# Performance work log

Hardware: AMD Instinct MI355X
Metric: run time of the kernel (lower is better)

The kernel has to match this reference:

```python
import jax, jax.numpy as jnp
import numpy as np

N_NODES = 100000
N_EDGES = 1600000


def setup_inputs() -> dict:
    key = jax.random.key(0)
    k1, k2, k3, k4 = jax.random.split(key, 4)
    x = jax.random.normal(k1, (N_NODES, 128), dtype=jnp.float32)
    edge_index = jax.random.randint(k2, (2, N_EDGES), 0, N_NODES, dtype=jnp.int64)
    # Glorot-ish init for weights
    W1 = jax.random.normal(k3, (128, 128), dtype=jnp.float32) * (1.0 / np.sqrt(128))
    b1 = jnp.zeros((128,), dtype=jnp.float32)
    W2 = jax.random.normal(k4, (128, 64), dtype=jnp.float32) * (1.0 / np.sqrt(128))
    b2 = jnp.zeros((64,), dtype=jnp.float32)
    return {"x": x, "edge_index": edge_index, "W1": W1, "b1": b1, "W2": W2, "b2": b2}


def _gcn_conv(x, src, dst, W, b):
    """PyG GCNConv: h = W x; symmetric deg^-1/2 norm over edges (incl. self-loops); scatter-add; + bias."""
    n = x.shape[0]
    h = x @ W  # [N, out]
    ones = jnp.ones(src.shape[0], dtype=h.dtype)
    deg = jax.ops.segment_sum(ones, dst, num_segments=n)  # in-degree incl self-loops
    dinv = jax.lax.rsqrt(jnp.maximum(deg, 1e-12))
    norm = dinv[src] * dinv[dst]  # [E+N]
    msg = h[src] * norm[:, None]  # [E+N, out] gather
    out = jax.ops.segment_sum(msg, dst, num_segments=n)  # scatter-add
    return out + b


def reference(x, edge_index, W1, b1, W2, b2):
    n = x.shape[0]
    loop = jnp.arange(n, dtype=edge_index.dtype)
    src = jnp.concatenate([edge_index[0], loop])  # add self-loops
    dst = jnp.concatenate([edge_index[1], loop])
    h = jax.nn.relu(_gcn_conv(x, src, dst, W1, b1))
    # dropout is identity in eval mode
    return _gcn_conv(h, src, dst, W2, b2)
```

## Files before the change

### kernel.cpp

```cpp
#include <hip/hip_runtime.h>
#include <hip/hip_bf16.h>

#define THREADS 256
#define BSHIFT 9
#define BIN_CHUNK 4096

typedef __attribute__((ext_vector_type(8))) short bf16x8;
typedef __attribute__((ext_vector_type(4))) float f32x4;


__device__ inline unsigned short f2bf(float f) {
    unsigned int u = __float_as_uint(f);
    unsigned int r = (u + 0x7fffu + ((u >> 16) & 1u)) >> 16;
    return (unsigned short)r;
}

__device__ inline unsigned int pack_bf2(float x, float y) {
    return (unsigned int)f2bf(x) | ((unsigned int)f2bf(y) << 16);
}

__device__ inline float2 bf2_to_f2(unsigned int u) {
    float2 r;
    r.x = __uint_as_float(u << 16);
    r.y = __uint_as_float(u & 0xffff0000u);
    return r;
}

__device__ inline unsigned short bf_relu(unsigned short v) {
    return (v & 0x8000u) ? (unsigned short)0 : v;
}

__device__ inline void accum_row(float* acc, uint4 v) {
    float2 a = bf2_to_f2(v.x), b = bf2_to_f2(v.y), c = bf2_to_f2(v.z), d = bf2_to_f2(v.w);
    acc[0] += a.x; acc[1] += a.y; acc[2] += b.x; acc[3] += b.y;
    acc[4] += c.x; acc[5] += c.y; acc[6] += d.x; acc[7] += d.y;
}


__global__ __launch_bounds__(256) void k_bin(const int* __restrict__ src,
                                             const int* __restrict__ dst,
                                             int* __restrict__ bcur,
                                             unsigned int* __restrict__ binned,
                                             int E, int NB, int cap) {
    __shared__ int bcnt[256];
    __shared__ int bres[256];
    int t = threadIdx.x;
    bcnt[t] = 0;
    __syncthreads();
    int base = blockIdx.x * BIN_CHUNK;
    int sv[16], dv[16];
#pragma unroll
    for (int i = 0; i < 16; ++i) {
        int e = base + t + i * 256;
        if (e < E) {
            sv[i] = src[e];
            dv[i] = dst[e];
            atomicAdd(&bcnt[dv[i] >> BSHIFT], 1);
        } else {
            dv[i] = -1;
        }
    }
    __syncthreads();
    if (t < NB) {
        int old = bcnt[t] ? atomicAdd(&bcur[t], bcnt[t]) : 0;
        bres[t] = t * cap + old;
    }
    __syncthreads();
#pragma unroll
    for (int i = 0; i < 16; ++i) {
        if (dv[i] >= 0) {
            int b = dv[i] >> BSHIFT;
            int pos = atomicAdd(&bres[b], 1);
            if (pos < (b + 1) * cap)
                binned[pos] = ((unsigned int)(dv[i] & 511) << 23) | (unsigned int)sv[i];
        }
    }
}

__global__ __launch_bounds__(256) void k_node_place(const unsigned int* __restrict__ binned,
                                                    const int* __restrict__ bcur, int cap,
                                                    int* __restrict__ rp,
                                                    int* __restrict__ deg,
                                                    float* __restrict__ dinv,
                                                    int* __restrict__ eperm, int N) {
    __shared__ int lc[512];
    __shared__ int s[256];
    int b = blockIdx.x;
    int t = threadIdx.x;
    int beg = b * cap;
    int end = beg + min(bcur[b], cap);
    int d0 = b << BSHIFT;
    lc[t] = 0;
    lc[t + 256] = 0;
    __syncthreads();
    for (int j = beg + t; j < end; j += 256) atomicAdd(&lc[binned[j] >> 23], 1);
    __syncthreads();
    int a = lc[2 * t], c = lc[2 * t + 1];
    int pair = a + c;
    s[t] = pair;
    __syncthreads();
    for (int off = 1; off < 256; off <<= 1) {
        int add = (t >= off) ? s[t - off] : 0;
        __syncthreads();
        s[t] += add;
        __syncthreads();
    }
    int excl = s[t] - pair;
    int st0 = beg + excl, st1 = st0 + a;
    int node0 = d0 + 2 * t;
    if (node0 < N) {
        rp[node0] = st0;
        deg[node0] = a;
        dinv[node0] = rsqrtf((float)a + 1.0f);
    }
    if (node0 + 1 < N) {
        rp[node0 + 1] = st1;
        deg[node0 + 1] = c;
        dinv[node0 + 1] = rsqrtf((float)c + 1.0f);
    }
    __syncthreads();
    lc[2 * t] = st0;
    lc[2 * t + 1] = st1;
    __syncthreads();
    for (int j = beg + t; j < end; j += 256) {
        unsigned int p = binned[j];
        int pos = atomicAdd(&lc[p >> 23], 1);
        eperm[pos] = (int)(p & 0x7fffffu);
    }
}


template <int N, bool ABF16_RELU>
__global__ __launch_bounds__(256) void k_gemm_mfma(const void* __restrict__ Av,
                                                   const float* __restrict__ W,
                                                   const float* __restrict__ dinv,
                                                   unsigned short* __restrict__ C, int M) {
    static_assert(N == 64 || N == 128, "N must be 64 or 128");
    constexpr int NT = N / 64;
    constexpr int KP = 136;
    __shared__ short As[64 * KP];
    __shared__ short Bs[N * KP];
    __shared__ float sDin[64];

    const int t = threadIdx.x;
    const int m0 = blockIdx.x * 64;

    {
        int ar = t >> 5;
        int ac = (t & 31) * 4;
#pragma unroll
        for (int rb = 0; rb < 64; rb += 8) {
            int lrow = rb + ar;
            int row = m0 + lrow;
            ushort4 sv = make_ushort4(0, 0, 0, 0);
            if (ABF16_RELU) {
                if (row < M) {
                    ushort4 u = *(const ushort4*)((const unsigned short*)Av + (size_t)row * 128 + ac);
                    sv.x = bf_relu(u.x); sv.y = bf_relu(u.y);
                    sv.z = bf_relu(u.z); sv.w = bf_relu(u.w);
                }
            } else {
                if (row < M) {
                    float4 v = *(const float4*)((const float*)Av + (size_t)row * 128 + ac);
                    sv.x = f2bf(v.x); sv.y = f2bf(v.y); sv.z = f2bf(v.z); sv.w = f2bf(v.w);
                }
            }
            *(ushort4*)&As[lrow * KP + ac] = sv;
        }
    }
    {
        constexpr int TPR = N / 4;
        constexpr int KPI = 256 / TPR;
        int bk = t / TPR;
        int bn = (t % TPR) * 4;
#pragma unroll
        for (int kb = 0; kb < 128; kb += KPI) {
            int k = kb + bk;
            float4 wv = *(const float4*)(W + (size_t)k * N + bn);
            Bs[(bn + 0) * KP + k] = f2bf(wv.x);
            Bs[(bn + 1) * KP + k] = f2bf(wv.y);
            Bs[(bn + 2) * KP + k] = f2bf(wv.z);
            Bs[(bn + 3) * KP + k] = f2bf(wv.w);
        }
    }
    if (t < 64) sDin[t] = (m0 + t < M) ? dinv[m0 + t] : 1.0f;
    __syncthreads();

    const int w = t >> 6;
    const int lane = t & 63;
    const int lm = lane & 15;
    const int qd = lane >> 4;
    const int n0w = w * 16 * NT;

    f32x4 acc[4][NT];
#pragma unroll
    for (int mi = 0; mi < 4; ++mi)
#pragma unroll
        for (int ni = 0; ni < NT; ++ni) acc[mi][ni] = (f32x4){0.f, 0.f, 0.f, 0.f};

#pragma unroll
    for (int ks = 0; ks < 4; ++ks) {
        bf16x8 a[4], b[NT];
#pragma unroll
        for (int mi = 0; mi < 4; ++mi)
            a[mi] = *(const bf16x8*)&As[(mi * 16 + lm) * KP + ks * 32 + qd * 8];
#pragma unroll
        for (int ni = 0; ni < NT; ++ni)
            b[ni] = *(const bf16x8*)&Bs[(n0w + ni * 16 + lm) * KP + ks * 32 + qd * 8];
#pragma unroll
        for (int mi = 0; mi < 4; ++mi)
#pragma unroll
            for (int ni = 0; ni < NT; ++ni)
                acc[mi][ni] = __builtin_amdgcn_mfma_f32_16x16x32_bf16(a[mi], b[ni], acc[mi][ni], 0, 0, 0);
    }

#pragma unroll
    for (int mi = 0; mi < 4; ++mi) {
#pragma unroll
        for (int ni = 0; ni < NT; ++ni) {
            int col = n0w + ni * 16 + lm;
#pragma unroll
            for (int r = 0; r < 4; ++r) {
                int lrow = mi * 16 + qd * 4 + r;
                int row = m0 + lrow;
                if (row < M) C[(size_t)row * N + col] = f2bf(sDin[lrow] * acc[mi][ni][r]);
            }
        }
    }
}


__global__ __launch_bounds__(256) void k_gather128(const int* __restrict__ rp,
                                                   const int* __restrict__ deg,
                                                   const int* __restrict__ eperm,
                                                   const float* __restrict__ dinv,
                                                   const uint4* __restrict__ h4,
                                                   const float* __restrict__ bias,
                                                   uint4* __restrict__ out4,
                                                   int n) {
    const int t = threadIdx.x;
    const int lane = t & 63;
    const int l16 = lane & 15;
    const int gbase = lane & 48;
    const int node = blockIdx.x * 16 + (t >> 6) * 4 + (lane >> 4);
    const bool valid = node < n;

    int beg = 0, end = 0;
    if (valid) {
        beg = rp[node];
        end = beg + deg[node];
    }

    float acc[8];
#pragma unroll
    for (int i = 0; i < 8; ++i) acc[i] = 0.f;
    if (valid) accum_row(acc, h4[(size_t)node * 16 + l16]);

    int j = beg;
    for (; j + 16 <= end; j += 16) {
        int ep = eperm[j + l16];
        int idx[16];
#pragma unroll
        for (int k = 0; k < 16; ++k) idx[k] = __shfl(ep, gbase + k);
        uint4 v[16];
#pragma unroll
        for (int k = 0; k < 16; ++k) v[k] = h4[(size_t)idx[k] * 16 + l16];
#pragma unroll
        for (int k = 0; k < 16; ++k) accum_row(acc, v[k]);
    }
    int cnt = end - j;
    if (cnt > 0) {
        int ep = eperm[j + (l16 < cnt ? l16 : cnt - 1)];
        int k = 0;
        for (; k + 4 <= cnt; k += 4) {
            int i0 = __shfl(ep, gbase + k);
            int i1 = __shfl(ep, gbase + k + 1);
            int i2 = __shfl(ep, gbase + k + 2);
            int i3 = __shfl(ep, gbase + k + 3);
            uint4 v0 = h4[(size_t)i0 * 16 + l16];
            uint4 v1 = h4[(size_t)i1 * 16 + l16];
            uint4 v2 = h4[(size_t)i2 * 16 + l16];
            uint4 v3 = h4[(size_t)i3 * 16 + l16];
            accum_row(acc, v0);
            accum_row(acc, v1);
            accum_row(acc, v2);
            accum_row(acc, v3);
        }
        for (; k < cnt; ++k) {
            int i0 = __shfl(ep, gbase + k);
            uint4 v0 = h4[(size_t)i0 * 16 + l16];
            accum_row(acc, v0);
        }
    }

    if (valid) {
        float dv = dinv[node];
        float4 b0 = ((const float4*)bias)[l16 * 2];
        float4 b1 = ((const float4*)bias)[l16 * 2 + 1];
        uint4 o;
        o.x = pack_bf2(dv * acc[0] + b0.x, dv * acc[1] + b0.y);
        o.y = pack_bf2(dv * acc[2] + b0.z, dv * acc[3] + b0.w);
        o.z = pack_bf2(dv * acc[4] + b1.x, dv * acc[5] + b1.y);
        o.w = pack_bf2(dv * acc[6] + b1.z, dv * acc[7] + b1.w);
        out4[(size_t)node * 16 + l16] = o;
    }
}

__global__ __launch_bounds__(256) void k_gather64(const int* __restrict__ rp,
                                                  const int* __restrict__ deg,
                                                  const int* __restrict__ eperm,
                                                  const float* __restrict__ dinv,
                                                  const uint4* __restrict__ h4,
                                                  const float* __restrict__ bias,
                                                  float* __restrict__ out, int n) {
    const int t = threadIdx.x;
    const int lane = t & 63;
    const int l8 = lane & 7;
    const int gbase = lane & 56;
    const int node = blockIdx.x * 32 + (t >> 6) * 8 + (lane >> 3);
    const bool valid = node < n;

    int beg = 0, end = 0;
    if (valid) {
        beg = rp[node];
        end = beg + deg[node];
    }

    float acc[8];
#pragma unroll
    for (int i = 0; i < 8; ++i) acc[i] = 0.f;
    if (valid) accum_row(acc, h4[(size_t)node * 8 + l8]);

    int j = beg;
    for (; j + 16 <= end; j += 16) {
        int ep0 = eperm[j + l8];
        int ep1 = eperm[j + 8 + l8];
        int idx[16];
#pragma unroll
        for (int k = 0; k < 8; ++k) idx[k] = __shfl(ep0, gbase + k);
#pragma unroll
        for (int k = 0; k < 8; ++k) idx[8 + k] = __shfl(ep1, gbase + k);
        uint4 v[16];
#pragma unroll
        for (int k = 0; k < 16; ++k) v[k] = h4[(size_t)idx[k] * 8 + l8];
#pragma unroll
        for (int k = 0; k < 16; ++k) accum_row(acc, v[k]);
    }
    int cnt = end - j;
    if (cnt >= 8) {
        int ep = eperm[j + l8];
        int idx[8];
#pragma unroll
        for (int k = 0; k < 8; ++k) idx[k] = __shfl(ep, gbase + k);
        uint4 v[8];
#pragma unroll
        for (int k = 0; k < 8; ++k) v[k] = h4[(size_t)idx[k] * 8 + l8];
#pragma unroll
        for (int k = 0; k < 8; ++k) accum_row(acc, v[k]);
        j += 8;
        cnt -= 8;
    }
    if (cnt > 0) {
        int ep = eperm[j + (l8 < cnt ? l8 : cnt - 1)];
        int k = 0;
        for (; k + 4 <= cnt; k += 4) {
            int i0 = __shfl(ep, gbase + k);
            int i1 = __shfl(ep, gbase + k + 1);
            int i2 = __shfl(ep, gbase + k + 2);
            int i3 = __shfl(ep, gbase + k + 3);
            uint4 v0 = h4[(size_t)i0 * 8 + l8];
            uint4 v1 = h4[(size_t)i1 * 8 + l8];
            uint4 v2 = h4[(size_t)i2 * 8 + l8];
            uint4 v3 = h4[(size_t)i3 * 8 + l8];
            accum_row(acc, v0);
            accum_row(acc, v1);
            accum_row(acc, v2);
            accum_row(acc, v3);
        }
        for (; k < cnt; ++k) {
            int i0 = __shfl(ep, gbase + k);
            uint4 v0 = h4[(size_t)i0 * 8 + l8];
            accum_row(acc, v0);
        }
    }

    if (valid) {
        float dv = dinv[node];
        float4 b0 = ((const float4*)bias)[l8 * 2];
        float4 b1 = ((const float4*)bias)[l8 * 2 + 1];
        float4 o0, o1;
        o0.x = dv * acc[0] + b0.x; o0.y = dv * acc[1] + b0.y;
        o0.z = dv * acc[2] + b0.z; o0.w = dv * acc[3] + b0.w;
        o1.x = dv * acc[4] + b1.x; o1.y = dv * acc[5] + b1.y;
        o1.z = dv * acc[6] + b1.z; o1.w = dv * acc[7] + b1.w;
        float4* orow = (float4*)(out + (size_t)node * 64);
        orow[l8 * 2] = o0;
        orow[l8 * 2 + 1] = o1;
    }
}


extern "C" void kernel_launch(void* const* d_in, const int* in_sizes, int n_in,
                              void* d_out, int out_size, void* d_ws, size_t ws_size,
                              hipStream_t stream) {
    const float* x  = (const float*)d_in[0];
    const int*   ei = (const int*)d_in[1];
    const float* W1 = (const float*)d_in[2];
    const float* b1 = (const float*)d_in[3];
    const float* W2 = (const float*)d_in[4];
    const float* b2 = (const float*)d_in[5];
    float* out = (float*)d_out;

    const int N = in_sizes[0] / 128;
    const int E = in_sizes[1] / 2;
    const int* src = ei;
    const int* dst = ei + E;
    const int NB = (N + 511) >> BSHIFT;
    const int cap = (E + NB - 1) / NB + ((E / NB) >> 2) + 1024;

    char* ws = (char*)d_ws;
    size_t off = 0;
    auto carve = [&](size_t bytes) -> void* {
        void* p = ws + off;
        off = (off + bytes + 255) & ~(size_t)255;
        return p;
    };
    float* dinv = (float*)carve((size_t)N * 4);
    int*   rp   = (int*)carve((size_t)N * 4);
    int*   deg  = (int*)carve((size_t)N * 4);
    int*   bcur = (int*)carve(256 * 4);
    unsigned int* binned = (unsigned int*)carve((size_t)NB * cap * 4);
    int*   eperm = (int*)carve((size_t)NB * cap * 4);
    unsigned short* h    = (unsigned short*)carve((size_t)N * 128 * 2);
    unsigned short* hagg = (unsigned short*)carve((size_t)N * 128 * 2);
    unsigned short* h2 = h;

    const int gMm = (N + 63) / 64;

    hipMemsetAsync(bcur, 0, 256 * sizeof(int), stream);
    k_bin<<<(E + BIN_CHUNK - 1) / BIN_CHUNK, THREADS, 0, stream>>>(src, dst, bcur, binned, E, NB, cap);
    k_node_place<<<NB, THREADS, 0, stream>>>(binned, bcur, cap, rp, deg, dinv, eperm, N);

    k_gemm_mfma<128, false><<<gMm, THREADS, 0, stream>>>(x, W1, dinv, h, N);
    k_gather128<<<(N + 15) / 16, THREADS, 0, stream>>>(rp, deg, eperm, dinv, (const uint4*)h, b1,
                                                       (uint4*)hagg, N);

    k_gemm_mfma<64, true><<<gMm, THREADS, 0, stream>>>(hagg, W2, dinv, h2, N);
    k_gather64<<<(N + 31) / 32, THREADS, 0, stream>>>(rp, deg, eperm, dinv, (const uint4*)h2, b2, out, N);
}
```

Before: 290.9 us.

## Fuse edge binning with GEMM1 and layer-1 gather with GEMM2

Edge binning and the first dense transform now share one launch, so GEMM1 no longer depends on the degree computation. The transform output is left unscaled, and the per-source dinv is applied inside the gather via a per-edge scale. The layer-1 aggregation, ReLU and bias now write into shared memory and feed the second MFMA GEMM directly. This removes the hagg round trip through global memory and a launch, but adds an extra dinv gather per edge and lowers gather parallelism, since each block handles 64 nodes in a serial loop of four.

```diff
diff --git a/kernel.cpp b/kernel.cpp
--- a/kernel.cpp
+++ b/kernel.cpp
@@ -4,6 +4,7 @@
 #define THREADS 256
 #define BSHIFT 9
 #define BIN_CHUNK 4096
+#define KP 136
 
 typedef __attribute__((ext_vector_type(8))) short bf16x8;
 typedef __attribute__((ext_vector_type(4))) float f32x4;
@@ -13,10 +14,6 @@
     unsigned int u = __float_as_uint(f);
     unsigned int r = (u + 0x7fffu + ((u >> 16) & 1u)) >> 16;
     return (unsigned short)r;
-}
-
-__device__ inline unsigned int pack_bf2(float x, float y) {
-    return (unsigned int)f2bf(x) | ((unsigned int)f2bf(y) << 16);
 }
 
 __device__ inline float2 bf2_to_f2(unsigned int u) {
@@ -26,53 +23,142 @@
     return r;
 }
 
-__device__ inline unsigned short bf_relu(unsigned short v) {
-    return (v & 0x8000u) ? (unsigned short)0 : v;
-}
-
 __device__ inline void accum_row(float* acc, uint4 v) {
     float2 a = bf2_to_f2(v.x), b = bf2_to_f2(v.y), c = bf2_to_f2(v.z), d = bf2_to_f2(v.w);
     acc[0] += a.x; acc[1] += a.y; acc[2] += b.x; acc[3] += b.y;
     acc[4] += c.x; acc[5] += c.y; acc[6] += d.x; acc[7] += d.y;
 }
 
-
-__global__ __launch_bounds__(256) void k_bin(const int* __restrict__ src,
-                                             const int* __restrict__ dst,
-                                             int* __restrict__ bcur,
-                                             unsigned int* __restrict__ binned,
-                                             int E, int NB, int cap) {
-    __shared__ int bcnt[256];
-    __shared__ int bres[256];
-    int t = threadIdx.x;
-    bcnt[t] = 0;
-    __syncthreads();
-    int base = blockIdx.x * BIN_CHUNK;
-    int sv[16], dv[16];
-#pragma unroll
-    for (int i = 0; i < 16; ++i) {
-        int e = base + t + i * 256;
-        if (e < E) {
-            sv[i] = src[e];
-            dv[i] = dst[e];
-            atomicAdd(&bcnt[dv[i] >> BSHIFT], 1);
-        } else {
-            dv[i] = -1;
-        }
-    }
-    __syncthreads();
-    if (t < NB) {
-        int old = bcnt[t] ? atomicAdd(&bcur[t], bcnt[t]) : 0;
-        bres[t] = t * cap + old;
-    }
-    __syncthreads();
-#pragma unroll
-    for (int i = 0; i < 16; ++i) {
-        if (dv[i] >= 0) {
-            int b = dv[i] >> BSHIFT;
-            int pos = atomicAdd(&bres[b], 1);
-            if (pos < (b + 1) * cap)
-                binned[pos] = ((unsigned int)(dv[i] & 511) << 23) | (unsigned int)sv[i];
+__device__ inline void accum_row_scaled(float* acc, uint4 v, float s) {
+    float2 a = bf2_to_f2(v.x), b = bf2_to_f2(v.y), c = bf2_to_f2(v.z), d = bf2_to_f2(v.w);
+    acc[0] = fmaf(s, a.x, acc[0]); acc[1] = fmaf(s, a.y, acc[1]);
+    acc[2] = fmaf(s, b.x, acc[2]); acc[3] = fmaf(s, b.y, acc[3]);
+    acc[4] = fmaf(s, c.x, acc[4]); acc[5] = fmaf(s, c.y, acc[5]);
+    acc[6] = fmaf(s, d.x, acc[6]); acc[7] = fmaf(s, d.y, acc[7]);
+}
+
+
+__global__ __launch_bounds__(256) void k_bin_gemm1(const int* __restrict__ src,
+                                                   const int* __restrict__ dst,
+                                                   int* __restrict__ bcur,
+                                                   unsigned int* __restrict__ binned,
+                                                   int E, int NB, int cap,
+                                                   const float* __restrict__ x,
+                                                   const float* __restrict__ W1,
+                                                   unsigned short* __restrict__ h,
+                                                   int M, int nbin) {
+    __shared__ __align__(16) char smem[64 * KP * 2 + 128 * KP * 2];
+    const int t = threadIdx.x;
+
+    if ((int)blockIdx.x < nbin) {
+        int* bcnt = (int*)smem;
+        int* bres = bcnt + 256;
+        bcnt[t] = 0;
+        __syncthreads();
+        int base = blockIdx.x * BIN_CHUNK;
+        int sv[16], dv[16];
+#pragma unroll
+        for (int i = 0; i < 16; ++i) {
+            int e = base + t + i * 256;
+            if (e < E) {
+                sv[i] = src[e];
+                dv[i] = dst[e];
+                atomicAdd(&bcnt[dv[i] >> BSHIFT], 1);
+            } else {
+                dv[i] = -1;
+            }
+        }
+        __syncthreads();
+        if (t < NB) {
+            int old = bcnt[t] ? atomicAdd(&bcur[t], bcnt[t]) : 0;
+            bres[t] = t * cap + old;
+        }
+        __syncthreads();
+#pragma unroll
+        for (int i = 0; i < 16; ++i) {
+            if (dv[i] >= 0) {
+                int b = dv[i] >> BSHIFT;
+                int pos = atomicAdd(&bres[b], 1);
+                if (pos < (b + 1) * cap)
+                    binned[pos] = ((unsigned int)(dv[i] & 511) << 23) | (unsigned int)sv[i];
+            }
+        }
+        return;
+    }
+
+    short* As = (short*)smem;
+    short* Bs = (short*)(smem + 64 * KP * 2);
+    const int m0 = ((int)blockIdx.x - nbin) * 64;
+
+    {
+        int ar = t >> 5;
+        int ac = (t & 31) * 4;
+#pragma unroll
+        for (int rb = 0; rb < 64; rb += 8) {
+            int lrow = rb + ar;
+            int row = m0 + lrow;
+            ushort4 sv = make_ushort4(0, 0, 0, 0);
+            if (row < M) {
+                float4 v = *(const float4*)(x + (size_t)row * 128 + ac);
+                sv.x = f2bf(v.x); sv.y = f2bf(v.y); sv.z = f2bf(v.z); sv.w = f2bf(v.w);
+            }
+            *(ushort4*)&As[lrow * KP + ac] = sv;
+        }
+    }
+    {
+        int bk = t / 32;
+        int bn = (t % 32) * 4;
+#pragma unroll
+        for (int kb = 0; kb < 128; kb += 8) {
+            int k = kb + bk;
+            float4 wv = *(const float4*)(W1 + (size_t)k * 128 + bn);
+            Bs[(bn + 0) * KP + k] = f2bf(wv.x);
+            Bs[(bn + 1) * KP + k] = f2bf(wv.y);
+            Bs[(bn + 2) * KP + k] = f2bf(wv.z);
+            Bs[(bn + 3) * KP + k] = f2bf(wv.w);
+        }
+    }
+    __syncthreads();
+
+    const int w = t >> 6;
+    const int lane = t & 63;
+    const int lm = lane & 15;
+    const int qd = lane >> 4;
+    const int n0w = w * 32;
+
+    f32x4 acc[4][2];
+#pragma unroll
+    for (int mi = 0; mi < 4; ++mi)
+#pragma unroll
+        for (int ni = 0; ni < 2; ++ni) acc[mi][ni] = (f32x4){0.f, 0.f, 0.f, 0.f};
+
+#pragma unroll
+    for (int ks = 0; ks < 4; ++ks) {
+        bf16x8 a[4], b[2];
+#pragma unroll
+        for (int mi = 0; mi < 4; ++mi)
+            a[mi] = *(const bf16x8*)&As[(mi * 16 + lm) * KP + ks * 32 + qd * 8];
+#pragma unroll
+        for (int ni = 0; ni < 2; ++ni)
+            b[ni] = *(const bf16x8*)&Bs[(n0w + ni * 16 + lm) * KP + ks * 32 + qd * 8];
+#pragma unroll
+        for (int mi = 0; mi < 4; ++mi)
+#pragma unroll
+            for (int ni = 0; ni < 2; ++ni)
+                acc[mi][ni] = __builtin_amdgcn_mfma_f32_16x16x32_bf16(a[mi], b[ni], acc[mi][ni], 0, 0, 0);
+    }
+
+#pragma unroll
+    for (int mi = 0; mi < 4; ++mi) {
+#pragma unroll
+        for (int ni = 0; ni < 2; ++ni) {
+            int col = n0w + ni * 16 + lm;
+#pragma unroll
+            for (int r = 0; r < 4; ++r) {
+                int lrow = mi * 16 + qd * 4 + r;
+                int row = m0 + lrow;
+                if (row < M) h[(size_t)row * 128 + col] = f2bf(acc[mi][ni][r]);
+            }
         }
     }
 }
@@ -130,179 +216,138 @@
 }
 
 
-template <int N, bool ABF16_RELU>
-__global__ __launch_bounds__(256) void k_gemm_mfma(const void* __restrict__ Av,
-                                                   const float* __restrict__ W,
-                                                   const float* __restrict__ dinv,
-                                                   unsigned short* __restrict__ C, int M) {
-    static_assert(N == 64 || N == 128, "N must be 64 or 128");
-    constexpr int NT = N / 64;
-    constexpr int KP = 136;
+__global__ __launch_bounds__(256) void k_gather_gemm2(const int* __restrict__ rp,
+                                                      const int* __restrict__ deg,
+                                                      const int* __restrict__ eperm,
+                                                      const float* __restrict__ dinv,
+                                                      const uint4* __restrict__ h4,
+                                                      const float* __restrict__ b1,
+                                                      const float* __restrict__ W2,
+                                                      unsigned short* __restrict__ h2,
+                                                      int n) {
     __shared__ short As[64 * KP];
-    __shared__ short Bs[N * KP];
+    __shared__ short Bs[64 * KP];
     __shared__ float sDin[64];
 
     const int t = threadIdx.x;
+    const int lane = t & 63;
+    const int l16 = lane & 15;
+    const int gbase = lane & 48;
     const int m0 = blockIdx.x * 64;
 
     {
-        int ar = t >> 5;
-        int ac = (t & 31) * 4;
-#pragma unroll
-        for (int rb = 0; rb < 64; rb += 8) {
-            int lrow = rb + ar;
-            int row = m0 + lrow;
-            ushort4 sv = make_ushort4(0, 0, 0, 0);
-            if (ABF16_RELU) {
-                if (row < M) {
-                    ushort4 u = *(const ushort4*)((const unsigned short*)Av + (size_t)row * 128 + ac);
-                    sv.x = bf_relu(u.x); sv.y = bf_relu(u.y);
-                    sv.z = bf_relu(u.z); sv.w = bf_relu(u.w);
-                }
-            } else {
-                if (row < M) {
-                    float4 v = *(const float4*)((const float*)Av + (size_t)row * 128 + ac);
-                    sv.x = f2bf(v.x); sv.y = f2bf(v.y); sv.z = f2bf(v.z); sv.w = f2bf(v.w);
-                }
-            }
-            *(ushort4*)&As[lrow * KP + ac] = sv;
-        }
-    }
-    {
-        constexpr int TPR = N / 4;
-        constexpr int KPI = 256 / TPR;
-        int bk = t / TPR;
-        int bn = (t % TPR) * 4;
-#pragma unroll
-        for (int kb = 0; kb < 128; kb += KPI) {
+        int bk = t / 16;
+        int bn = (t % 16) * 4;
+#pragma unroll
+        for (int kb = 0; kb < 128; kb += 16) {
             int k = kb + bk;
-            float4 wv = *(const float4*)(W + (size_t)k * N + bn);
+            float4 wv = *(const float4*)(W2 + (size_t)k * 64 + bn);
             Bs[(bn + 0) * KP + k] = f2bf(wv.x);
             Bs[(bn + 1) * KP + k] = f2bf(wv.y);
             Bs[(bn + 2) * KP + k] = f2bf(wv.z);
             Bs[(bn + 3) * KP + k] = f2bf(wv.w);
         }
     }
-    if (t < 64) sDin[t] = (m0 + t < M) ? dinv[m0 + t] : 1.0f;
+    if (t < 64) sDin[t] = (m0 + t < n) ? dinv[m0 + t] : 1.0f;
+
+#pragma unroll 1
+    for (int r = 0; r < 4; ++r) {
+        const int lrow = r * 16 + ((t >> 6) << 2) + (lane >> 4);
+        const int node = m0 + lrow;
+        const bool valid = node < n;
+
+        int beg = 0, end = 0;
+        float dv_self = 0.f;
+        if (valid) {
+            beg = rp[node];
+            end = beg + deg[node];
+            dv_self = dinv[node];
+        }
+
+        float acc[8];
+#pragma unroll
+        for (int i = 0; i < 8; ++i) acc[i] = 0.f;
+        if (valid) accum_row_scaled(acc, h4[(size_t)node * 16 + l16], dv_self);
+
+        for (int j = beg; j < end; j += 16) {
+            int cnt = end - j;
+            if (cnt > 16) cnt = 16;
+            int ep = eperm[j + (l16 < cnt ? l16 : cnt - 1)];
+            float dvv = dinv[ep];
+            int k = 0;
+            for (; k + 4 <= cnt; k += 4) {
+                int i0 = __shfl(ep, gbase + k);
+                int i1 = __shfl(ep, gbase + k + 1);
+                int i2 = __shfl(ep, gbase + k + 2);
+                int i3 = __shfl(ep, gbase + k + 3);
+                float d0 = __shfl(dvv, gbase + k);
+                float d1 = __shfl(dvv, gbase + k + 1);
+                float d2 = __shfl(dvv, gbase + k + 2);
+                float d3 = __shfl(dvv, gbase + k + 3);
+                uint4 v0 = h4[(size_t)i0 * 16 + l16];
+                uint4 v1 = h4[(size_t)i1 * 16 + l16];
+                uint4 v2 = h4[(size_t)i2 * 16 + l16];
+                uint4 v3 = h4[(size_t)i3 * 16 + l16];
+                accum_row_scaled(acc, v0, d0);
+                accum_row_scaled(acc, v1, d1);
+                accum_row_scaled(acc, v2, d2);
+                accum_row_scaled(acc, v3, d3);
+            }
+            for (; k < cnt; ++k) {
+                int i0 = __shfl(ep, gbase + k);
+                float d0 = __shfl(dvv, gbase + k);
+                uint4 v0 = h4[(size_t)i0 * 16 + l16];
+                accum_row_scaled(acc, v0, d0);
+            }
+        }
+
+        float4 bb0 = ((const float4*)b1)[l16 * 2];
+        float4 bb1 = ((const float4*)b1)[l16 * 2 + 1];
+        float o0 = fmaxf(fmaf(dv_self, acc[0], bb0.x), 0.f);
+        float o1 = fmaxf(fmaf(dv_self, acc[1], bb0.y), 0.f);
+        float o2 = fmaxf(fmaf(dv_self, acc[2], bb0.z), 0.f);
+        float o3 = fmaxf(fmaf(dv_self, acc[3], bb0.w), 0.f);
+        float o4 = fmaxf(fmaf(dv_self, acc[4], bb1.x), 0.f);
+        float o5 = fmaxf(fmaf(dv_self, acc[5], bb1.y), 0.f);
+        float o6 = fmaxf(fmaf(dv_self, acc[6], bb1.z), 0.f);
+        float o7 = fmaxf(fmaf(dv_self, acc[7], bb1.w), 0.f);
+        ushort4 s0 = make_ushort4(f2bf(o0), f2bf(o1), f2bf(o2), f2bf(o3));
+        ushort4 s1 = make_ushort4(f2bf(o4), f2bf(o5), f2bf(o6), f2bf(o7));
+        *(ushort4*)&As[lrow * KP + l16 * 8] = s0;
+        *(ushort4*)&As[lrow * KP + l16 * 8 + 4] = s1;
+    }
     __syncthreads();
 
     const int w = t >> 6;
-    const int lane = t & 63;
     const int lm = lane & 15;
     const int qd = lane >> 4;
-    const int n0w = w * 16 * NT;
-
-    f32x4 acc[4][NT];
-#pragma unroll
-    for (int mi = 0; mi < 4; ++mi)
-#pragma unroll
-        for (int ni = 0; ni < NT; ++ni) acc[mi][ni] = (f32x4){0.f, 0.f, 0.f, 0.f};
+    const int n0w = w * 16;
+
+    f32x4 c4[4];
+#pragma unroll
+    for (int mi = 0; mi < 4; ++mi) c4[mi] = (f32x4){0.f, 0.f, 0.f, 0.f};
 
 #pragma unroll
     for (int ks = 0; ks < 4; ++ks) {
-        bf16x8 a[4], b[NT];
+        bf16x8 a[4], b;
 #pragma unroll
         for (int mi = 0; mi < 4; ++mi)
             a[mi] = *(const bf16x8*)&As[(mi * 16 + lm) * KP + ks * 32 + qd * 8];
-#pragma unroll
-        for (int ni = 0; ni < NT; ++ni)
-            b[ni] = *(const bf16x8*)&Bs[(n0w + ni * 16 + lm) * KP + ks * 32 + qd * 8];
+        b = *(const bf16x8*)&Bs[(n0w + lm) * KP + ks * 32 + qd * 8];
 #pragma unroll
         for (int mi = 0; mi < 4; ++mi)
-#pragma unroll
-            for (int ni = 0; ni < NT; ++ni)
-                acc[mi][ni] = __builtin_amdgcn_mfma_f32_16x16x32_bf16(a[mi], b[ni], acc[mi][ni], 0, 0, 0);
+            c4[mi] = __builtin_amdgcn_mfma_f32_16x16x32_bf16(a[mi], b, c4[mi], 0, 0, 0);
     }
 
 #pragma unroll
     for (int mi = 0; mi < 4; ++mi) {
-#pragma unroll
-        for (int ni = 0; ni < NT; ++ni) {
-            int col = n0w + ni * 16 + lm;
-#pragma unroll
-            for (int r = 0; r < 4; ++r) {
-                int lrow = mi * 16 + qd * 4 + r;
-                int row = m0 + lrow;
-                if (row < M) C[(size_t)row * N + col] = f2bf(sDin[lrow] * acc[mi][ni][r]);
-            }
-        }
-    }
-}
-
-
-__global__ __launch_bounds__(256) void k_gather128(const int* __restrict__ rp,
-                                                   const int* __restrict__ deg,
-                                                   const int* __restrict__ eperm,
-                                                   const float* __restrict__ dinv,
-                                                   const uint4* __restrict__ h4,
-                                                   const float* __restrict__ bias,
-                                                   uint4* __restrict__ out4,
-                                                   int n) {
-    const int t = threadIdx.x;
-    const int lane = t & 63;
-    const int l16 = lane & 15;
-    const int gbase = lane & 48;
-    const int node = blockIdx.x * 16 + (t >> 6) * 4 + (lane >> 4);
-    const bool valid = node < n;
-
-    int beg = 0, end = 0;
-    if (valid) {
-        beg = rp[node];
-        end = beg + deg[node];
-    }
-
-    float acc[8];
-#pragma unroll
-    for (int i = 0; i < 8; ++i) acc[i] = 0.f;
-    if (valid) accum_row(acc, h4[(size_t)node * 16 + l16]);
-
-    int j = beg;
-    for (; j + 16 <= end; j += 16) {
-        int ep = eperm[j + l16];
-        int idx[16];
-#pragma unroll
-        for (int k = 0; k < 16; ++k) idx[k] = __shfl(ep, gbase + k);
-        uint4 v[16];
-#pragma unroll
-        for (int k = 0; k < 16; ++k) v[k] = h4[(size_t)idx[k] * 16 + l16];
-#pragma unroll
-        for (int k = 0; k < 16; ++k) accum_row(acc, v[k]);
-    }
-    int cnt = end - j;
-    if (cnt > 0) {
-        int ep = eperm[j + (l16 < cnt ? l16 : cnt - 1)];
-        int k = 0;
-        for (; k + 4 <= cnt; k += 4) {
-            int i0 = __shfl(ep, gbase + k);
-            int i1 = __shfl(ep, gbase + k + 1);
-            int i2 = __shfl(ep, gbase + k + 2);
-            int i3 = __shfl(ep, gbase + k + 3);
-            uint4 v0 = h4[(size_t)i0 * 16 + l16];
-            uint4 v1 = h4[(size_t)i1 * 16 + l16];
-            uint4 v2 = h4[(size_t)i2 * 16 + l16];
-            uint4 v3 = h4[(size_t)i3 * 16 + l16];
-            accum_row(acc, v0);
-            accum_row(acc, v1);
-            accum_row(acc, v2);
-            accum_row(acc, v3);
-        }
-        for (; k < cnt; ++k) {
-            int i0 = __shfl(ep, gbase + k);
-            uint4 v0 = h4[(size_t)i0 * 16 + l16];
-            accum_row(acc, v0);
-        }
-    }
-
-    if (valid) {
-        float dv = dinv[node];
-        float4 b0 = ((const float4*)bias)[l16 * 2];
-        float4 b1 = ((const float4*)bias)[l16 * 2 + 1];
-        uint4 o;
-        o.x = pack_bf2(dv * acc[0] + b0.x, dv * acc[1] + b0.y);
-        o.y = pack_bf2(dv * acc[2] + b0.z, dv * acc[3] + b0.w);
-        o.z = pack_bf2(dv * acc[4] + b1.x, dv * acc[5] + b1.y);
-        o.w = pack_bf2(dv * acc[6] + b1.z, dv * acc[7] + b1.w);
-        out4[(size_t)node * 16 + l16] = o;
+        int col = n0w + lm;
+#pragma unroll
+        for (int r = 0; r < 4; ++r) {
+            int lrow = mi * 16 + qd * 4 + r;
+            int row = m0 + lrow;
+            if (row < n) h2[(size_t)row * 64 + col] = f2bf(sDin[lrow] * c4[mi][r]);
+        }
     }
 }
 
@@ -431,20 +476,18 @@
     int*   bcur = (int*)carve(256 * 4);
     unsigned int* binned = (unsigned int*)carve((size_t)NB * cap * 4);
     int*   eperm = (int*)carve((size_t)NB * cap * 4);
-    unsigned short* h    = (unsigned short*)carve((size_t)N * 128 * 2);
-    unsigned short* hagg = (unsigned short*)carve((size_t)N * 128 * 2);
-    unsigned short* h2 = h;
+    unsigned short* h  = (unsigned short*)carve((size_t)N * 128 * 2);
+    unsigned short* h2 = (unsigned short*)carve((size_t)N * 128 * 2);
 
     const int gMm = (N + 63) / 64;
+    const int nbin = (E + BIN_CHUNK - 1) / BIN_CHUNK;
 
     hipMemsetAsync(bcur, 0, 256 * sizeof(int), stream);
-    k_bin<<<(E + BIN_CHUNK - 1) / BIN_CHUNK, THREADS, 0, stream>>>(src, dst, bcur, binned, E, NB, cap);
+    k_bin_gemm1<<<nbin + gMm, THREADS, 0, stream>>>(src, dst, bcur, binned, E, NB, cap,
+                                                    x, W1, h, N, nbin);
     k_node_place<<<NB, THREADS, 0, stream>>>(binned, bcur, cap, rp, deg, dinv, eperm, N);
 
-    k_gemm_mfma<128, false><<<gMm, THREADS, 0, stream>>>(x, W1, dinv, h, N);
-    k_gather128<<<(N + 15) / 16, THREADS, 0, stream>>>(rp, deg, eperm, dinv, (const uint4*)h, b1,
-                                                       (uint4*)hagg, N);
-
-    k_gemm_mfma<64, true><<<gMm, THREADS, 0, stream>>>(hagg, W2, dinv, h2, N);
+    k_gather_gemm2<<<gMm, THREADS, 0, stream>>>(rp, deg, eperm, dinv, (const uint4*)h, b1, W2, h2, N);
+
     k_gather64<<<(N + 31) / 32, THREADS, 0, stream>>>(rp, deg, eperm, dinv, (const uint4*)h2, b2, out, N);
 }
```

Result: faster. 275.0 us (-5.5%).
